# Kernel tuning notes

Measured on AMD Instinct MI355X. Metric: run time of the kernel, lower is better.

## Reference

```python
import jax, jax.numpy as jnp
import numpy as np

B, L, D = 4, 4096, 1024


def setup_inputs() -> dict:
    key = jax.random.key(0)
    ks = jax.random.split(key, 10)
    s = 1.0 / np.sqrt(D)  # torch Linear default init scale
    return {
        "x": jax.random.normal(ks[0], (B, L, D), dtype=jnp.float32),
        "hidden": jax.random.normal(ks[1], (B, D), dtype=jnp.float32),
        "W_ln_z": jax.random.uniform(ks[2], (D, D), jnp.float32, -s, s),
        "b_ln_z": jax.random.uniform(ks[3], (D,), jnp.float32, -s, s),
        "W_dt": jax.random.uniform(ks[4], (D, D), jnp.float32, -s, s),
        "b_dt": jax.random.uniform(ks[5], (D,), jnp.float32, -s, s),
        "W_y": jax.random.uniform(ks[6], (D, D), jnp.float32, -s, s),
        "b_y": jax.random.uniform(ks[7], (D,), jnp.float32, -s, s),
        "W_g": jax.random.uniform(ks[8], (D, D), jnp.float32, -s, s),
        "b_g": jax.random.uniform(ks[9], (D,), jnp.float32, -s, s),
    }


def reference(x, hidden, W_ln_z, b_ln_z, W_dt, b_dt, W_y, b_y, W_g, b_g):
    # Linear projections (torch Linear: x @ W.T + b)
    z_pre = x @ W_ln_z.T + b_ln_z          # (B, L, D)
    dt_pre = x @ W_dt.T + b_dt             # (B, L, D)

    # -softplus(-u) == log_sigmoid(u)
    ln_z = jax.nn.log_sigmoid(z_pre)       # ln z
    ln_da = jax.nn.log_sigmoid(dt_pre)     # ln(delta*a)
    ln_z_da = ln_z + ln_da
    ln_o_da = jax.nn.log_sigmoid(-dt_pre)  # -softplus(dt_pre)

    ln_o_da_cumsum = jnp.cumsum(ln_o_da, axis=1)
    # log-space parallel scan: h_t = sum_{s<=t} z_s*da_s * prod_{s<r<=t} o_da_r
    lcse = jax.lax.cumlogsumexp(ln_z_da - ln_o_da_cumsum, axis=1)
    h_inner = jnp.exp(lcse + ln_o_da_cumsum)                       # (B, L, D)
    h_cross = jnp.exp(ln_o_da_cumsum) * hidden[:, None, :]         # (B, L, D)
    h = h_inner + h_cross

    gate = jax.nn.silu(x @ W_g.T + b_g)
    y = (h @ W_y.T + b_y) * gate
    return y, h
```

## Files before the change

kernel.cpp:

```cpp
#include <hip/hip_runtime.h>


#define BDIM 4
#define LDIM 4096
#define DDIM 1024
#define MROWS (BDIM * LDIM)
#define KDIM 1024
#define NPROJ 3072
#define NCHUNK 64
#define LCHUNK 64

typedef __attribute__((ext_vector_type(8))) short short8v;
typedef __attribute__((ext_vector_type(4))) float f32x4;

__device__ __forceinline__ float bf2f(short u) {
    union { float f; unsigned int i; } v;
    v.i = ((unsigned int)(unsigned short)u) << 16;
    return v.f;
}
__device__ __forceinline__ short f2bf(float f) {
    union { float f; unsigned int i; } v; v.f = f;
    unsigned int r = v.i + 0x7FFFu + ((v.i >> 16) & 1u);
    return (short)(r >> 16);
}
__device__ __forceinline__ float sigf(float x) { return 1.f / (1.f + __expf(-x)); }

__global__ void cast_f32_bf16(const float* __restrict__ src, short* __restrict__ dst, int n4) {
    int i = blockIdx.x * blockDim.x + threadIdx.x;
    int stride = gridDim.x * blockDim.x;
    for (; i < n4; i += stride) {
        float4 v = reinterpret_cast<const float4*>(src)[i];
        short4 o;
        o.x = f2bf(v.x); o.y = f2bf(v.y); o.z = f2bf(v.z); o.w = f2bf(v.w);
        reinterpret_cast<short4*>(dst)[i] = o;
    }
}


#define STAGE(arr, gbase, half, kofs)                                              \
  do {                                                                             \
    _Pragma("unroll")                                                              \
    for (int _i = 0; _i < 2; ++_i) {                                               \
      int _c = _i * 512 + tid;                                                     \
      int _row = _c >> 3, _g = _c & 7;                                             \
      int _gsw = _g ^ (_row & 7);                                                  \
      __builtin_amdgcn_global_load_lds(                                            \
        (const __attribute__((address_space(1))) void*)(                           \
            (gbase) + (size_t)((half) * 128 + _row) * K + (kofs) + _gsw * 8),      \
        (__attribute__((address_space(3))) void*)(                                 \
            &arr[(_i * 512 + wid * 64) * 8]),                                      \
        16, 0, 0);                                                                 \
    }                                                                              \
  } while (0)

#define LDA4(dst, arr)                                                             \
  _Pragma("unroll")                                                                \
  for (int _m = 0; _m < 4; ++_m) {                                                 \
    int _r = _m * 32 + wm * 16 + lrow;                                             \
    _Pragma("unroll")                                                              \
    for (int _kk = 0; _kk < 2; ++_kk)                                              \
      dst[_m][_kk] = *(const short8v*)&arr[_r * 64 +                               \
                       (((_kk * 4 + kq) ^ (lrow & 7)) * 8)];                       \
  }

#define LDB2(dst, arr)                                                             \
  _Pragma("unroll")                                                                \
  for (int _n = 0; _n < 2; ++_n) {                                                 \
    int _r = _n * 64 + wn * 16 + lrow;                                             \
    _Pragma("unroll")                                                              \
    for (int _kk = 0; _kk < 2; ++_kk)                                              \
      dst[_n][_kk] = *(const short8v*)&arr[_r * 64 +                               \
                       (((_kk * 4 + kq) ^ (lrow & 7)) * 8)];                       \
  }

#define MFMAQ(mi0, ni0, afr, bfr)                                                  \
  __builtin_amdgcn_s_setprio(1);                                                   \
  _Pragma("unroll")                                                                \
  for (int _kk = 0; _kk < 2; ++_kk)                                                \
    _Pragma("unroll")                                                              \
    for (int _m = 0; _m < 4; ++_m)                                                 \
      _Pragma("unroll")                                                            \
      for (int _n = 0; _n < 2; ++_n)                                               \
        acc[(mi0) + _m][(ni0) + _n] = __builtin_amdgcn_mfma_f32_16x16x32_bf16(     \
            afr[_m][_kk], bfr[_n][_kk], acc[(mi0) + _m][(ni0) + _n], 0, 0, 0);     \
  __builtin_amdgcn_s_setprio(0);

#define BARB()       __builtin_amdgcn_s_barrier()
#define BAR_VM4()    asm volatile("s_waitcnt vmcnt(4)\ns_barrier" ::: "memory")
#define BAR_VM0()    asm volatile("s_waitcnt vmcnt(0)\ns_barrier" ::: "memory")

template<int OUT_BF16, int HAS_GATE>
__global__ __launch_bounds__(512, 2) void gemm256(
    const short* __restrict__ A, const short* __restrict__ Bm,
    const float* __restrict__ bias, void* __restrict__ Cv,
    int M, int N, int K,
    const short* __restrict__ gate, int ldg)
{
    __shared__ short As0h0[8192], As0h1[8192], As1h0[8192], As1h1[8192];
    __shared__ short Bs0h0[8192], Bs0h1[8192], Bs1h0[8192], Bs1h1[8192];

    const int tid  = threadIdx.x;
    const int lane = tid & 63;
    const int wid  = tid >> 6;
    const int wm   = wid >> 2;
    const int wn   = wid & 3;
    const int lrow = lane & 15;
    const int kq   = lane >> 4;

    const int gx  = gridDim.x;
    const int nwg = gx * gridDim.y;
    int flat = blockIdx.y * gx + blockIdx.x;
    if ((nwg & 7) == 0) { int q = nwg >> 3; flat = (flat & 7) * q + (flat >> 3); }
    const int m0 = (flat / gx) * 256;
    const int n0 = (flat % gx) * 256;

    const short* Abase = A + (size_t)m0 * K;
    const short* Bbase = Bm + (size_t)n0 * K;

    f32x4 acc[8][4];
#pragma unroll
    for (int i = 0; i < 8; ++i)
#pragma unroll
        for (int j = 0; j < 4; ++j)
            acc[i][j] = (f32x4){0.f, 0.f, 0.f, 0.f};

    STAGE(As0h0, Abase, 0, 0);
    STAGE(As0h1, Abase, 1, 0);
    STAGE(Bs0h0, Bbase, 0, 0);
    STAGE(Bs0h1, Bbase, 1, 0);
    STAGE(As1h0, Abase, 0, 64);
    STAGE(Bs1h0, Bbase, 0, 64);
    BAR_VM4();

    const int NT = K / 64;
    for (int t = 0; t < NT; t += 2) {
        const int k1 = (t + 1) * 64, k2 = (t + 2) * 64, k3 = (t + 3) * 64;
        const bool more = (t + 2) < NT;
        short8v af[4][2], b0[2][2], b1[2][2];

        LDA4(af, As0h0) LDB2(b0, Bs0h0)
        STAGE(As1h1, Abase, 1, k1);
        BARB(); MFMAQ(0, 0, af, b0) BARB();

        LDB2(b1, Bs0h1)
        STAGE(Bs1h1, Bbase, 1, k1);
        BARB(); MFMAQ(0, 2, af, b1) BARB();

        LDA4(af, As0h1)
        if (more) STAGE(As0h0, Abase, 0, k2);
        BARB(); MFMAQ(4, 2, af, b1) BARB();

        if (more) STAGE(Bs0h0, Bbase, 0, k2);
        BARB(); MFMAQ(4, 0, af, b0)
        if (more) { BAR_VM4(); } else { BAR_VM0(); }

        LDA4(af, As1h0) LDB2(b0, Bs1h0)
        if (more) STAGE(As0h1, Abase, 1, k2);
        BARB(); MFMAQ(0, 0, af, b0) BARB();

        LDB2(b1, Bs1h1)
        if (more) STAGE(Bs0h1, Bbase, 1, k2);
        BARB(); MFMAQ(0, 2, af, b1) BARB();

        LDA4(af, As1h1)
        if (more) STAGE(As1h0, Abase, 0, k3);
        BARB(); MFMAQ(4, 2, af, b1) BARB();

        if (more) STAGE(Bs1h0, Bbase, 0, k3);
        BARB(); MFMAQ(4, 0, af, b0)
        if (more) { BAR_VM4(); } else { BARB(); }
    }

    const int lr4 = (lane >> 4) * 4;
#pragma unroll
    for (int mi = 0; mi < 8; ++mi) {
        int rowb = m0 + mi * 32 + wm * 16 + lr4;
#pragma unroll
        for (int ni = 0; ni < 4; ++ni) {
            int col = n0 + ni * 64 + wn * 16 + lrow;
            float bv = bias[col];
#pragma unroll
            for (int r = 0; r < 4; ++r) {
                int row = rowb + r;
                float val = acc[mi][ni][r] + bv;
                if (HAS_GATE) {
                    float g = bf2f(gate[(size_t)row * ldg + col]);
                    val *= g * sigf(g);
                }
                if (OUT_BF16)
                    ((short*)Cv)[(size_t)row * N + col] = f2bf(val);
                else
                    ((float*)Cv)[(size_t)row * N + col] = val;
            }
        }
    }
}

__global__ __launch_bounds__(1024) void chunk_reduce(
    const short* __restrict__ pre, float* __restrict__ sA, float* __restrict__ sBv)
{
    const int d = threadIdx.x;
    const int c = blockIdx.x;
    const int b = blockIdx.y;
    float Aacc = 1.f, Bacc = 0.f;
    size_t base = ((size_t)(b * LDIM) + c * LCHUNK) * NPROJ;
    for (int i = 0; i < LCHUNK; ++i) {
        float z  = bf2f(pre[base + d]);
        float dt = bf2f(pre[base + DDIM + d]);
        float e  = __expf(-dt);
        float r  = 1.f / (1.f + e);
        float oda = e * r;
        float zda = sigf(z) * r;
        Bacc = zda + oda * Bacc;
        Aacc *= oda;
        base += NPROJ;
    }
    int idx = ((b * NCHUNK + c) << 10) + d;
    sA[idx]  = Aacc;
    sBv[idx] = Bacc;
}

__global__ __launch_bounds__(1024) void chunk_prefix(
    const float* __restrict__ sA, const float* __restrict__ sBv,
    const float* __restrict__ hidden, float* __restrict__ sI)
{
    const int d = threadIdx.x;
    const int b = blockIdx.x;
    float h = hidden[b * DDIM + d];
    for (int c = 0; c < NCHUNK; ++c) {
        int idx = ((b * NCHUNK + c) << 10) + d;
        sI[idx] = h;
        h = sBv[idx] + sA[idx] * h;
    }
}

__global__ __launch_bounds__(1024) void chunk_apply(
    const short* __restrict__ pre, const float* __restrict__ sI,
    float* __restrict__ hout, short* __restrict__ hbf)
{
    const int d = threadIdx.x;
    const int c = blockIdx.x;
    const int b = blockIdx.y;
    float h = sI[((b * NCHUNK + c) << 10) + d];
    size_t base  = ((size_t)(b * LDIM) + c * LCHUNK) * NPROJ;
    size_t obase = ((size_t)(b * LDIM) + c * LCHUNK) * DDIM + d;
    for (int i = 0; i < LCHUNK; ++i) {
        float z  = bf2f(pre[base + d]);
        float dt = bf2f(pre[base + DDIM + d]);
        float e  = __expf(-dt);
        float r  = 1.f / (1.f + e);
        float oda = e * r;
        float zda = sigf(z) * r;
        h = zda + oda * h;
        hout[obase] = h;
        hbf[obase]  = f2bf(h);
        base += NPROJ;
        obase += DDIM;
    }
}

extern "C" void kernel_launch(void* const* d_in, const int* in_sizes, int n_in,
                              void* d_out, int out_size, void* d_ws, size_t ws_size,
                              hipStream_t stream) {
    const float* x      = (const float*)d_in[0];
    const float* hidden = (const float*)d_in[1];
    const float* W_ln_z = (const float*)d_in[2];
    const float* b_ln_z = (const float*)d_in[3];
    const float* W_dt   = (const float*)d_in[4];
    const float* b_dt   = (const float*)d_in[5];
    const float* W_y    = (const float*)d_in[6];
    const float* b_y    = (const float*)d_in[7];
    const float* W_g    = (const float*)d_in[8];
    const float* b_g    = (const float*)d_in[9];

    char* ws = (char*)d_ws;
    short* x_bf   = (short*)(ws + 0);
    short* Wcat   = (short*)(ws + 33554432);
    short* Wy_bf  = (short*)(ws + 39845888);
    float* biascat= (float*)(ws + 41943040);
    short* pre    = (short*)(ws + 41955328);
    float* sA     = (float*)(ws + 142618624);
    float* sBv    = (float*)(ws + 143667200);
    float* sI     = (float*)(ws + 144715776);

    cast_f32_bf16<<<2048, 256, 0, stream>>>(x, x_bf, (MROWS * KDIM) / 4);
    cast_f32_bf16<<<1024, 256, 0, stream>>>(W_ln_z, Wcat,                (DDIM * KDIM) / 4);
    cast_f32_bf16<<<1024, 256, 0, stream>>>(W_dt,   Wcat + DDIM * KDIM,  (DDIM * KDIM) / 4);
    cast_f32_bf16<<<1024, 256, 0, stream>>>(W_g,    Wcat + 2 * DDIM * KDIM, (DDIM * KDIM) / 4);
    cast_f32_bf16<<<1024, 256, 0, stream>>>(W_y,    Wy_bf,               (DDIM * KDIM) / 4);

    hipMemcpyAsync(biascat,            b_ln_z, DDIM * sizeof(float), hipMemcpyDeviceToDevice, stream);
    hipMemcpyAsync(biascat + DDIM,     b_dt,   DDIM * sizeof(float), hipMemcpyDeviceToDevice, stream);
    hipMemcpyAsync(biascat + 2 * DDIM, b_g,    DDIM * sizeof(float), hipMemcpyDeviceToDevice, stream);

    gemm256<1, 0><<<dim3(NPROJ / 256, MROWS / 256), 512, 0, stream>>>(
        x_bf, Wcat, biascat, pre, MROWS, NPROJ, KDIM, nullptr, 0);

    float* y_out = (float*)d_out;
    float* h_out = (float*)d_out + (size_t)MROWS * DDIM;
    short* h_bf  = x_bf;
    chunk_reduce<<<dim3(NCHUNK, BDIM), 1024, 0, stream>>>(pre, sA, sBv);
    chunk_prefix<<<dim3(BDIM), 1024, 0, stream>>>(sA, sBv, hidden, sI);
    chunk_apply<<<dim3(NCHUNK, BDIM), 1024, 0, stream>>>(pre, sI, h_out, h_bf);

    gemm256<0, 1><<<dim3(DDIM / 256, MROWS / 256), 512, 0, stream>>>(
        h_bf, Wy_bf, b_y, y_out, MROWS, DDIM, KDIM, pre + 2 * DDIM, NPROJ);
}
```

Baseline: 264.6 us.

## Merge weight cast launches and halve barriers in the GEMM main loop

The four separate weight-cast launches become one kernel that selects the source matrix by segment. This works because Wy_bf sits directly after Wcat in the workspace. The bf16 GEMM main loop now loads both B fragments together and issues paired MFMA groups and paired LDS stages between fewer block barriers, which cuts synchronisation and launch overhead. Holding the second B fragment in registers earlier raises register pressure, and the changed interleaving of global-to-LDS staging with MFMA may alter latency hiding.

```diff
diff --git a/kernel.cpp b/kernel.cpp
--- a/kernel.cpp
+++ b/kernel.cpp
@@ -34,6 +34,18 @@
         o.x = f2bf(v.x); o.y = f2bf(v.y); o.z = f2bf(v.z); o.w = f2bf(v.w);
         reinterpret_cast<short4*>(dst)[i] = o;
     }
+}
+
+__global__ void cast4_f32_bf16(const float* __restrict__ s0, const float* __restrict__ s1,
+                               const float* __restrict__ s2, const float* __restrict__ s3,
+                               short* __restrict__ dst) {
+    int i = blockIdx.x * blockDim.x + threadIdx.x;
+    int seg = i >> 18, off = i & ((1 << 18) - 1);
+    const float* s = (seg == 0) ? s0 : (seg == 1) ? s1 : (seg == 2) ? s2 : s3;
+    float4 v = reinterpret_cast<const float4*>(s)[off];
+    short4 o;
+    o.x = f2bf(v.x); o.y = f2bf(v.y); o.z = f2bf(v.z); o.w = f2bf(v.w);
+    reinterpret_cast<short4*>(dst)[i] = o;
 }
 
 
@@ -138,36 +150,23 @@
         const bool more = (t + 2) < NT;
         short8v af[4][2], b0[2][2], b1[2][2];
 
-        LDA4(af, As0h0) LDB2(b0, Bs0h0)
+        LDA4(af, As0h0) LDB2(b0, Bs0h0) LDB2(b1, Bs0h1)
         STAGE(As1h1, Abase, 1, k1);
-        BARB(); MFMAQ(0, 0, af, b0) BARB();
-
-        LDB2(b1, Bs0h1)
         STAGE(Bs1h1, Bbase, 1, k1);
-        BARB(); MFMAQ(0, 2, af, b1) BARB();
+        BARB(); MFMAQ(0, 0, af, b0) MFMAQ(0, 2, af, b1) BARB();
 
         LDA4(af, As0h1)
-        if (more) STAGE(As0h0, Abase, 0, k2);
-        BARB(); MFMAQ(4, 2, af, b1) BARB();
-
-        if (more) STAGE(Bs0h0, Bbase, 0, k2);
-        BARB(); MFMAQ(4, 0, af, b0)
+        if (more) { STAGE(As0h0, Abase, 0, k2); STAGE(Bs0h0, Bbase, 0, k2); }
+        BARB(); MFMAQ(4, 2, af, b1) MFMAQ(4, 0, af, b0)
         if (more) { BAR_VM4(); } else { BAR_VM0(); }
 
-        LDA4(af, As1h0) LDB2(b0, Bs1h0)
-        if (more) STAGE(As0h1, Abase, 1, k2);
-        BARB(); MFMAQ(0, 0, af, b0) BARB();
-
-        LDB2(b1, Bs1h1)
-        if (more) STAGE(Bs0h1, Bbase, 1, k2);
-        BARB(); MFMAQ(0, 2, af, b1) BARB();
+        LDA4(af, As1h0) LDB2(b0, Bs1h0) LDB2(b1, Bs1h1)
+        if (more) { STAGE(As0h1, Abase, 1, k2); STAGE(Bs0h1, Bbase, 1, k2); }
+        BARB(); MFMAQ(0, 0, af, b0) MFMAQ(0, 2, af, b1) BARB();
 
         LDA4(af, As1h1)
-        if (more) STAGE(As1h0, Abase, 0, k3);
-        BARB(); MFMAQ(4, 2, af, b1) BARB();
-
-        if (more) STAGE(Bs1h0, Bbase, 0, k3);
-        BARB(); MFMAQ(4, 0, af, b0)
+        if (more) { STAGE(As1h0, Abase, 0, k3); STAGE(Bs1h0, Bbase, 0, k3); }
+        BARB(); MFMAQ(4, 2, af, b1) MFMAQ(4, 0, af, b0)
         if (more) { BAR_VM4(); } else { BARB(); }
     }
 
@@ -284,10 +283,7 @@
     float* sI     = (float*)(ws + 144715776);
 
     cast_f32_bf16<<<2048, 256, 0, stream>>>(x, x_bf, (MROWS * KDIM) / 4);
-    cast_f32_bf16<<<1024, 256, 0, stream>>>(W_ln_z, Wcat,                (DDIM * KDIM) / 4);
-    cast_f32_bf16<<<1024, 256, 0, stream>>>(W_dt,   Wcat + DDIM * KDIM,  (DDIM * KDIM) / 4);
-    cast_f32_bf16<<<1024, 256, 0, stream>>>(W_g,    Wcat + 2 * DDIM * KDIM, (DDIM * KDIM) / 4);
-    cast_f32_bf16<<<1024, 256, 0, stream>>>(W_y,    Wy_bf,               (DDIM * KDIM) / 4);
+    cast4_f32_bf16<<<4096, 256, 0, stream>>>(W_ln_z, W_dt, W_g, W_y, Wcat);
 
     hipMemcpyAsync(biascat,            b_ln_z, DDIM * sizeof(float), hipMemcpyDeviceToDevice, stream);
     hipMemcpyAsync(biascat + DDIM,     b_dt,   DDIM * sizeof(float), hipMemcpyDeviceToDevice, stream);
```

Result: slower. 281.1 us (+6.2%).
